# Performance work log

Hardware: AMD Instinct MI355X
Metric: run time of the kernel (lower is better)

## Reference

```python
import jax, jax.numpy as jnp
import numpy as np

H, W = 8, 8
N = 1 + H * W          # 65 tokens (cls + patches)
DIM = 128
HEADS = 8
DH = 32
INNER = HEADS * DH     # 256
B = 64
EPS = 1e-5


def setup_inputs() -> dict:
    key = jax.random.key(0)
    ks = jax.random.split(key, 7)
    x = jax.random.normal(ks[0], (B, N, DIM), dtype=jnp.float32)
    gamma = jnp.ones((DIM,), jnp.float32)
    beta = jnp.zeros((DIM,), jnp.float32)
    # kaiming_uniform-ish init scale for linear weights
    s_qk = float(np.sqrt(1.0 / DIM))
    Wqk = jax.random.uniform(ks[1], (DIM, 2 * INNER), jnp.float32, -s_qk, s_qk)
    # per-(query, key)-position value weights: [n, n, dim, inner]
    Wv = jax.random.uniform(ks[2], (N, N, DIM, INNER), jnp.float32, -s_qk, s_qk)
    s_o = float(np.sqrt(1.0 / INNER))
    Wout = jax.random.uniform(ks[3], (INNER, DIM), jnp.float32, -s_o, s_o)
    bout = jax.random.uniform(ks[4], (DIM,), jnp.float32, -s_o, s_o)
    return {"x": x, "gamma": gamma, "beta": beta, "Wqk": Wqk, "Wv": Wv,
            "Wout": Wout, "bout": bout}


def reference(x, gamma, beta, Wqk, Wv, Wout, bout):
    b, n, d = x.shape
    # LayerNorm
    mu = jnp.mean(x, axis=-1, keepdims=True)
    var = jnp.mean(jnp.square(x - mu), axis=-1, keepdims=True)
    xn = (x - mu) / jnp.sqrt(var + EPS) * gamma + beta
    # q, k projections
    qk = xn @ Wqk                               # [b, n, 2*inner]
    q, k = jnp.split(qk, 2, axis=-1)
    q = q.reshape(b, n, HEADS, DH).transpose(0, 2, 1, 3)  # [b, h, n, dh]
    k = k.reshape(b, n, HEADS, DH).transpose(0, 2, 1, 3)
    scale = DH ** -0.5
    dots = jnp.einsum('bhnd,bhmd->bhnm', q, k) * scale
    attn = jax.nn.softmax(dots, axis=-1)        # [b, h, n, m]
    # per-(n,m) value: v[b,n,m] = xn[b,n] @ Wv[n,m]  -> [b, n, m, inner]
    v = jnp.einsum('bnd,nmde->bnme', xn, Wv)
    v = v.reshape(b, n, n, HEADS, DH)           # [b, n, m, h, dh]
    # weighted sum over keys m
    out = jnp.einsum('bhnm,bnmhd->bnhd', attn, v).reshape(b, n, INNER)
    return out @ Wout + bout
```

## Files before the change

### kernel.cpp

```cpp
#include <hip/hip_runtime.h>

#define EPS 1e-5f

typedef __attribute__((ext_vector_type(8))) short short8;
typedef __attribute__((ext_vector_type(4))) float float4v;

__device__ __forceinline__ unsigned short f2bf(float x) {
  unsigned int u = __builtin_bit_cast(unsigned int, x);
  u += 0x7fffu + ((u >> 16) & 1u);
  return (unsigned short)(u >> 16);
}
__device__ __forceinline__ float bf2f(unsigned short h) {
  unsigned int u = ((unsigned int)h) << 16;
  return __builtin_bit_cast(float, u);
}

__global__ __launch_bounds__(256) void ln_kernel(
    const float* __restrict__ x, const float* __restrict__ gamma,
    const float* __restrict__ beta, float* __restrict__ xn,
    float* __restrict__ inner) {
  {
    const int zi = blockIdx.x * 1024 + threadIdx.x * 4;
    float4 z; z.x = 0.f; z.y = 0.f; z.z = 0.f; z.w = 0.f;
    *(float4*)(inner + zi) = z;
  }
  const int row = blockIdx.x * 4 + (threadIdx.x >> 6);
  const int lane = threadIdx.x & 63;
  const float2 v = ((const float2*)(x + (size_t)row * 128))[lane];
  float s = v.x + v.y;
#pragma unroll
  for (int off = 1; off < 64; off <<= 1) s += __shfl_xor(s, off);
  const float mu = s * (1.f / 128.f);
  const float dx = v.x - mu, dy = v.y - mu;
  float qv = dx * dx + dy * dy;
#pragma unroll
  for (int off = 1; off < 64; off <<= 1) qv += __shfl_xor(qv, off);
  const float rstd = 1.f / sqrtf(qv * (1.f / 128.f) + EPS);
  const float2 g = ((const float2*)gamma)[lane];
  const float2 be = ((const float2*)beta)[lane];
  float2 o;
  o.x = dx * rstd * g.x + be.x;
  o.y = dy * rstd * g.y + be.y;
  ((float2*)(xn + (size_t)row * 128))[lane] = o;
}

__global__ __launch_bounds__(256) void qk_kernel(
    const float* __restrict__ xn, const float* __restrict__ Wqk,
    float* __restrict__ qk) {
  __shared__ float xsx[32][130];
  __shared__ float wsx[128][68];
  const int t = threadIdx.x;
  const int r0 = blockIdx.x * 32, c0 = blockIdx.y * 64;
  for (int i = t; i < 32 * 32; i += 256) {
    int r = i >> 5, c = (i & 31) << 2;
    float4 v = *(const float4*)(xn + (size_t)(r0 + r) * 128 + c);
    float* dst = &xsx[r][c];
    dst[0] = v.x; dst[1] = v.y; dst[2] = v.z; dst[3] = v.w;
  }
  for (int i = t; i < 128 * 16; i += 256) {
    int k = i >> 4, c = (i & 15) << 2;
    *(float4*)&wsx[k][c] = *(const float4*)(Wqk + (size_t)k * 512 + c0 + c);
  }
  __syncthreads();
  const int rr = (t >> 4) * 2, cc = (t & 15) * 4;
  float acc[2][4] = {{0.f, 0.f, 0.f, 0.f}, {0.f, 0.f, 0.f, 0.f}};
  for (int k = 0; k < 128; k++) {
    float4 wv4 = *(const float4*)&wsx[k][cc];
    float x0 = xsx[rr][k], x1 = xsx[rr + 1][k];
    acc[0][0] += x0 * wv4.x; acc[0][1] += x0 * wv4.y;
    acc[0][2] += x0 * wv4.z; acc[0][3] += x0 * wv4.w;
    acc[1][0] += x1 * wv4.x; acc[1][1] += x1 * wv4.y;
    acc[1][2] += x1 * wv4.z; acc[1][3] += x1 * wv4.w;
  }
#pragma unroll
  for (int r = 0; r < 2; r++) {
    float4 o;
    o.x = acc[r][0]; o.y = acc[r][1]; o.z = acc[r][2]; o.w = acc[r][3];
    *(float4*)(qk + (size_t)(r0 + rr + r) * 512 + c0 + cc) = o;
  }
}

__global__ __launch_bounds__(256) void softmax_kernel(
    const float* __restrict__ qk, float* __restrict__ attn) {
  const int b = blockIdx.x >> 3, h = blockIdx.x & 7;
  __shared__ float qs[65][33];
  __shared__ float ks[65][33];
  __shared__ float dotsS[65][66];
  __shared__ float rsum[65];
  const int t = threadIdx.x;
  for (int i = t; i < 65 * 32; i += 256) {
    int n = i >> 5, d = i & 31;
    size_t base = ((size_t)b * 65 + n) * 512 + h * 32 + d;
    qs[n][d] = qk[base];
    ks[n][d] = qk[base + 256];
  }
  __syncthreads();
  const float scale = 0.17677669529663687f;
  for (int i = t; i < 65 * 65; i += 256) {
    int n = i / 65, mm = i - n * 65;
    float s = 0.f;
#pragma unroll
    for (int d = 0; d < 32; d++) s += qs[n][d] * ks[mm][d];
    dotsS[n][mm] = s * scale;
  }
  __syncthreads();
  if (t < 65) {
    float mx = -1e30f;
    for (int mm = 0; mm < 65; mm++) mx = fmaxf(mx, dotsS[t][mm]);
    float sum = 0.f;
    for (int mm = 0; mm < 65; mm++) {
      float e = __expf(dotsS[t][mm] - mx);
      dotsS[t][mm] = e;
      sum += e;
    }
    rsum[t] = 1.f / sum;
  }
  __syncthreads();
  const size_t obase = ((size_t)b * 8 + h) * 65 * 65;
  for (int i = t; i < 65 * 65; i += 256) {
    int n = i / 65;
    attn[obase + i] = dotsS[n][i - n * 65] * rsum[n];
  }
}

__global__ __launch_bounds__(256, 4) void attnv_kernel(
    const float* __restrict__ xn, const float* __restrict__ attn,
    const float* __restrict__ Wv, float* __restrict__ inner) {
  __shared__ __align__(16) char sbuf[33280];
  __shared__ float attnL[17 * 65];
  float* xs = (float*)sbuf;
  unsigned short* wvb = (unsigned short*)sbuf;

  const int nq = blockIdx.x >> 3, h = blockIdx.x & 7;
  const int mc = blockIdx.y;
  const int ms = (mc == 0) ? 0 : (17 + (mc - 1) * 16);
  const int cnt = (mc == 0) ? 17 : 16;

  const int t = threadIdx.x, lane = t & 63, w = t >> 6;
  const int boff = w * 16;
  const int er = lane & 15, q = lane >> 4;

  const int e = t & 31;
  const int d0 = (t >> 5) * 16;
  const int kc0 = d0 >> 3;
  const float* wbase = Wv + (size_t)nq * 65 * 32768 + (size_t)ms * 32768
                          + (size_t)h * 32 + e;

  float stg[16];
  {
    const float* p = wbase + (size_t)d0 * 256;
#pragma unroll
    for (int i = 0; i < 16; i++) stg[i] = __builtin_nontemporal_load(p + (size_t)i * 256);
  }

  for (int i = t; i < cnt * 64; i += 256) {
    int mloc = i >> 6, b = i & 63;
    attnL[mloc * 65 + b] =
        attn[(((size_t)b * 8 + h) * 65 + nq) * 65 + ms + mloc];
  }
  for (int i = t; i < 64 * 32; i += 256) {
    int b = i >> 5, c = (i & 31) << 2;
    float4 v = *(const float4*)(xn + ((size_t)b * 65 + nq) * 128 + c);
    float* dst = xs + b * 130 + c;
    dst[0] = v.x; dst[1] = v.y; dst[2] = v.z; dst[3] = v.w;
  }
  __syncthreads();

  short8 ah[4], al[4];
  {
    const int arow = boff + er;
#pragma unroll
    for (int s = 0; s < 4; s++) {
#pragma unroll
      for (int j = 0; j < 8; j++) {
        float xv = xs[arow * 130 + s * 32 + q * 8 + j];
        unsigned short hi = f2bf(xv);
        ah[s][j] = (short)hi;
        al[s][j] = (short)f2bf(xv - bf2f(hi));
      }
    }
  }
  __syncthreads();

  {
    short8 w0, w1;
#pragma unroll
    for (int j = 0; j < 8; j++) {
      w0[j] = (short)f2bf(stg[j]);
      w1[j] = (short)f2bf(stg[8 + j]);
    }
    *(short8*)&wvb[e * 128 + ((kc0 ^ (e & 15)) << 3)] = w0;
    *(short8*)&wvb[e * 128 + (((kc0 + 1) ^ (e & 15)) << 3)] = w1;
  }
  __syncthreads();

  float4v acc0 = {0.f, 0.f, 0.f, 0.f}, acc1 = {0.f, 0.f, 0.f, 0.f};

  for (int i = 0; i < cnt; i++) {
    const int cur = i & 1;
    if (i + 1 < cnt) {
      const float* p = wbase + (size_t)(i + 1) * 32768 + (size_t)d0 * 256;
#pragma unroll
      for (int j = 0; j < 16; j++) stg[j] = __builtin_nontemporal_load(p + (size_t)j * 256);
    }
    const unsigned short* wb = wvb + cur * 4096;
    float4v P0 = {0.f, 0.f, 0.f, 0.f}, P1 = {0.f, 0.f, 0.f, 0.f};
    __builtin_amdgcn_s_setprio(1);
#pragma unroll
    for (int s = 0; s < 4; s++) {
      const int kc = 4 * s + q;
      short8 b0 = *(const short8*)&wb[er * 128 + ((kc ^ er) << 3)];
      short8 b1 = *(const short8*)&wb[(er + 16) * 128 + ((kc ^ er) << 3)];
      P0 = __builtin_amdgcn_mfma_f32_16x16x32_bf16(ah[s], b0, P0, 0, 0, 0);
      P1 = __builtin_amdgcn_mfma_f32_16x16x32_bf16(ah[s], b1, P1, 0, 0, 0);
      P0 = __builtin_amdgcn_mfma_f32_16x16x32_bf16(al[s], b0, P0, 0, 0, 0);
      P1 = __builtin_amdgcn_mfma_f32_16x16x32_bf16(al[s], b1, P1, 0, 0, 0);
    }
    __builtin_amdgcn_s_setprio(0);
    {
      const float* ap = attnL + i * 65 + boff + q * 4;
#pragma unroll
      for (int r = 0; r < 4; r++) {
        float av = ap[r];
        acc0[r] += av * P0[r];
        acc1[r] += av * P1[r];
      }
    }
    if (i + 1 < cnt) {
      short8 w0, w1;
#pragma unroll
      for (int j = 0; j < 8; j++) {
        w0[j] = (short)f2bf(stg[j]);
        w1[j] = (short)f2bf(stg[8 + j]);
      }
      unsigned short* wbw = wvb + (1 - cur) * 4096;
      *(short8*)&wbw[e * 128 + ((kc0 ^ (e & 15)) << 3)] = w0;
      *(short8*)&wbw[e * 128 + (((kc0 + 1) ^ (e & 15)) << 3)] = w1;
    }
    __syncthreads();
  }

#pragma unroll
  for (int r = 0; r < 4; r++) {
    int b = boff + q * 4 + r;
    size_t o = ((size_t)b * 65 + nq) * 256 + h * 32;
    atomicAdd(inner + o + er, acc0[r]);
    atomicAdd(inner + o + 16 + er, acc1[r]);
  }
}

__global__ __launch_bounds__(256) void outproj_kernel(
    const float* __restrict__ inner, const float* __restrict__ Wout,
    const float* __restrict__ bout, float* __restrict__ out) {
  __shared__ float isx[16][258];
  __shared__ float wsx[64][132];
  const int t = threadIdx.x;
  const int r0 = blockIdx.x * 16;
  for (int i = t; i < 16 * 64; i += 256) {
    int r = i >> 6, c = (i & 63) << 2;
    float4 v = *(const float4*)(inner + (size_t)(r0 + r) * 256 + c);
    float* dst = &isx[r][c];
    dst[0] = v.x; dst[1] = v.y; dst[2] = v.z; dst[3] = v.w;
  }
  const int rr = (t >> 5) * 2, cc = (t & 31) * 4;
  float acc[2][4] = {{0.f, 0.f, 0.f, 0.f}, {0.f, 0.f, 0.f, 0.f}};
  for (int kc = 0; kc < 4; kc++) {
    __syncthreads();
    for (int i = t; i < 64 * 32; i += 256) {
      int k = i >> 5, c = (i & 31) << 2;
      *(float4*)&wsx[k][c] = *(const float4*)(Wout + (size_t)(kc * 64 + k) * 128 + c);
    }
    __syncthreads();
#pragma unroll 8
    for (int k = 0; k < 64; k++) {
      float4 wv4 = *(const float4*)&wsx[k][cc];
      float x0 = isx[rr][kc * 64 + k];
      float x1 = isx[rr + 1][kc * 64 + k];
      acc[0][0] += x0 * wv4.x; acc[0][1] += x0 * wv4.y;
      acc[0][2] += x0 * wv4.z; acc[0][3] += x0 * wv4.w;
      acc[1][0] += x1 * wv4.x; acc[1][1] += x1 * wv4.y;
      acc[1][2] += x1 * wv4.z; acc[1][3] += x1 * wv4.w;
    }
  }
  float4 bb = *(const float4*)(bout + cc);
#pragma unroll
  for (int r = 0; r < 2; r++) {
    float4 o;
    o.x = acc[r][0] + bb.x; o.y = acc[r][1] + bb.y;
    o.z = acc[r][2] + bb.z; o.w = acc[r][3] + bb.w;
    *(float4*)(out + (size_t)(r0 + rr + r) * 128 + cc) = o;
  }
}

extern "C" void kernel_launch(void* const* d_in, const int* in_sizes, int n_in,
                              void* d_out, int out_size, void* d_ws, size_t ws_size,
                              hipStream_t stream) {
  const float* x     = (const float*)d_in[0];
  const float* gamma = (const float*)d_in[1];
  const float* beta  = (const float*)d_in[2];
  const float* Wqk   = (const float*)d_in[3];
  const float* Wv    = (const float*)d_in[4];
  const float* Wout  = (const float*)d_in[5];
  const float* bout  = (const float*)d_in[6];
  float* out = (float*)d_out;
  float* ws  = (float*)d_ws;

  float* xn    = ws;
  float* qk    = ws + 532480;
  float* attn  = ws + 2662400;
  float* inner = ws + 4825600;

  ln_kernel<<<1040, 256, 0, stream>>>(x, gamma, beta, xn, inner);
  qk_kernel<<<dim3(130, 8), 256, 0, stream>>>(xn, Wqk, qk);
  softmax_kernel<<<512, 256, 0, stream>>>(qk, attn);
  attnv_kernel<<<dim3(520, 4), 256, 0, stream>>>(xn, attn, Wv, inner);
  outproj_kernel<<<260, 256, 0, stream>>>(inner, Wout, bout, out);
}
```

Before: 774.1 us.

## Restructure attn-v kernel so each block covers all heads for one query

Each attn-v block now handles one query position across all 8 heads, instead of one (query, head) pair, using 512 threads and a 16-way split over keys. Each Wv slice is fetched as contiguous 1KB rows of 256 floats rather than 128-byte pieces, and the converted xn fragments are reused across all heads. Every thread keeps 64 loads in flight to deepen the prefetch of the bandwidth-bound Wv stream. In exchange it uses 128KB of LDS per block and many more registers per thread, which limits occupancy to about one block per CU and risks register spilling.

```diff
diff --git a/kernel.cpp b/kernel.cpp
--- a/kernel.cpp
+++ b/kernel.cpp
@@ -123,42 +123,62 @@
   }
 }
 
-__global__ __launch_bounds__(256, 4) void attnv_kernel(
+__global__ __launch_bounds__(512, 2) void attnv_kernel(
     const float* __restrict__ xn, const float* __restrict__ attn,
     const float* __restrict__ Wv, float* __restrict__ inner) {
-  __shared__ __align__(16) char sbuf[33280];
-  __shared__ float attnL[17 * 65];
+  __shared__ __align__(16) char sbuf[131072];
+  __shared__ float attnL[5 * 8 * 64];
   float* xs = (float*)sbuf;
   unsigned short* wvb = (unsigned short*)sbuf;
 
-  const int nq = blockIdx.x >> 3, h = blockIdx.x & 7;
+  const int nq = blockIdx.x;
   const int mc = blockIdx.y;
-  const int ms = (mc == 0) ? 0 : (17 + (mc - 1) * 16);
-  const int cnt = (mc == 0) ? 17 : 16;
-
-  const int t = threadIdx.x, lane = t & 63, w = t >> 6;
-  const int boff = w * 16;
+  const int ms = (mc * 65) >> 4;
+  const int cnt = (((mc + 1) * 65) >> 4) - ms;
+
+  const int t = threadIdx.x;
+  const int lane = t & 63;
+  const int w = t >> 6;
   const int er = lane & 15, q = lane >> 4;
-
-  const int e = t & 31;
-  const int d0 = (t >> 5) * 16;
-  const int kc0 = d0 >> 3;
-  const float* wbase = Wv + (size_t)nq * 65 * 32768 + (size_t)ms * 32768
-                          + (size_t)h * 32 + e;
-
-  float stg[16];
-  {
-    const float* p = wbase + (size_t)d0 * 256;
-#pragma unroll
-    for (int i = 0; i < 16; i++) stg[i] = __builtin_nontemporal_load(p + (size_t)i * 256);
-  }
-
-  for (int i = t; i < cnt * 64; i += 256) {
-    int mloc = i >> 6, b = i & 63;
-    attnL[mloc * 65 + b] =
-        attn[(((size_t)b * 8 + h) * 65 + nq) * 65 + ms + mloc];
-  }
-  for (int i = t; i < 64 * 32; i += 256) {
+  const int rg = w & 1, cg = w >> 1;
+
+  const int eS = t & 255;
+  const int dS0 = (t >> 8) << 6;
+  const float* wq = Wv + ((size_t)nq * 65 + ms) * 32768 + (size_t)dS0 * 256 + eS;
+
+  float stg[64];
+
+#define ISSUE(mm) do {                                                        \
+    const float* p_ = wq + (size_t)(mm) * 32768;                              \
+    _Pragma("unroll")                                                         \
+    for (int i_ = 0; i_ < 64; i_++)                                           \
+      stg[i_] = __builtin_nontemporal_load(p_ + (size_t)i_ * 256);            \
+  } while (0)
+
+#define CONVWRITE(buf) do {                                                   \
+    unsigned short* wb_ = wvb + (size_t)(buf) * 32768 + eS * 128;             \
+    const int cb_ = (t >> 8) << 3;                                            \
+    _Pragma("unroll")                                                         \
+    for (int jj_ = 0; jj_ < 8; jj_++) {                                       \
+      short8 pk_;                                                             \
+      _Pragma("unroll")                                                       \
+      for (int j_ = 0; j_ < 8; j_++) pk_[j_] = (short)f2bf(stg[jj_ * 8 + j_]);\
+      *(short8*)&wb_[((cb_ + jj_) ^ (eS & 15)) << 3] = pk_;                   \
+    }                                                                         \
+  } while (0)
+
+  ISSUE(0);
+
+  const int tot = cnt << 9;
+  for (int i = t; i < tot; i += 512) {
+    int mloc = i % cnt;
+    int rest = i / cnt;
+    int h = rest & 7;
+    int b = rest >> 3;
+    attnL[(mloc * 8 + h) * 64 + b] =
+        attn[(((size_t)(b * 8 + h) * 65) + nq) * 65 + ms + mloc];
+  }
+  for (int i = t; i < 64 * 32; i += 512) {
     int b = i >> 5, c = (i & 31) << 2;
     float4 v = *(const float4*)(xn + ((size_t)b * 65 + nq) * 128 + c);
     float* dst = xs + b * 130 + c;
@@ -166,86 +186,84 @@
   }
   __syncthreads();
 
-  short8 ah[4], al[4];
-  {
-    const int arow = boff + er;
+  short8 ah[2][4], al[2][4];
+#pragma unroll
+  for (int rt = 0; rt < 2; rt++) {
+    const int arow = rg * 32 + rt * 16 + er;
 #pragma unroll
     for (int s = 0; s < 4; s++) {
 #pragma unroll
       for (int j = 0; j < 8; j++) {
         float xv = xs[arow * 130 + s * 32 + q * 8 + j];
         unsigned short hi = f2bf(xv);
-        ah[s][j] = (short)hi;
-        al[s][j] = (short)f2bf(xv - bf2f(hi));
+        ah[rt][s][j] = (short)hi;
+        al[rt][s][j] = (short)f2bf(xv - bf2f(hi));
       }
     }
   }
   __syncthreads();
 
-  {
-    short8 w0, w1;
-#pragma unroll
-    for (int j = 0; j < 8; j++) {
-      w0[j] = (short)f2bf(stg[j]);
-      w1[j] = (short)f2bf(stg[8 + j]);
-    }
-    *(short8*)&wvb[e * 128 + ((kc0 ^ (e & 15)) << 3)] = w0;
-    *(short8*)&wvb[e * 128 + (((kc0 + 1) ^ (e & 15)) << 3)] = w1;
-  }
-  __syncthreads();
-
-  float4v acc0 = {0.f, 0.f, 0.f, 0.f}, acc1 = {0.f, 0.f, 0.f, 0.f};
+  CONVWRITE(0);
+  __syncthreads();
+
+  float4v acc[2][4];
+#pragma unroll
+  for (int rt = 0; rt < 2; rt++)
+#pragma unroll
+    for (int ct = 0; ct < 4; ct++)
+      acc[rt][ct] = (float4v){0.f, 0.f, 0.f, 0.f};
 
   for (int i = 0; i < cnt; i++) {
-    const int cur = i & 1;
-    if (i + 1 < cnt) {
-      const float* p = wbase + (size_t)(i + 1) * 32768 + (size_t)d0 * 256;
-#pragma unroll
-      for (int j = 0; j < 16; j++) stg[j] = __builtin_nontemporal_load(p + (size_t)j * 256);
-    }
-    const unsigned short* wb = wvb + cur * 4096;
-    float4v P0 = {0.f, 0.f, 0.f, 0.f}, P1 = {0.f, 0.f, 0.f, 0.f};
+    if (i + 1 < cnt) ISSUE(i + 1);
+    const unsigned short* wb = wvb + (size_t)(i & 1) * 32768;
+    float4v P[2][4];
+#pragma unroll
+    for (int rt = 0; rt < 2; rt++)
+#pragma unroll
+      for (int ct = 0; ct < 4; ct++)
+        P[rt][ct] = (float4v){0.f, 0.f, 0.f, 0.f};
     __builtin_amdgcn_s_setprio(1);
 #pragma unroll
     for (int s = 0; s < 4; s++) {
       const int kc = 4 * s + q;
-      short8 b0 = *(const short8*)&wb[er * 128 + ((kc ^ er) << 3)];
-      short8 b1 = *(const short8*)&wb[(er + 16) * 128 + ((kc ^ er) << 3)];
-      P0 = __builtin_amdgcn_mfma_f32_16x16x32_bf16(ah[s], b0, P0, 0, 0, 0);
-      P1 = __builtin_amdgcn_mfma_f32_16x16x32_bf16(ah[s], b1, P1, 0, 0, 0);
-      P0 = __builtin_amdgcn_mfma_f32_16x16x32_bf16(al[s], b0, P0, 0, 0, 0);
-      P1 = __builtin_amdgcn_mfma_f32_16x16x32_bf16(al[s], b1, P1, 0, 0, 0);
+#pragma unroll
+      for (int ct = 0; ct < 4; ct++) {
+        short8 bf = *(const short8*)&wb[(cg * 64 + ct * 16 + er) * 128 + ((kc ^ er) << 3)];
+        P[0][ct] = __builtin_amdgcn_mfma_f32_16x16x32_bf16(ah[0][s], bf, P[0][ct], 0, 0, 0);
+        P[0][ct] = __builtin_amdgcn_mfma_f32_16x16x32_bf16(al[0][s], bf, P[0][ct], 0, 0, 0);
+        P[1][ct] = __builtin_amdgcn_mfma_f32_16x16x32_bf16(ah[1][s], bf, P[1][ct], 0, 0, 0);
+        P[1][ct] = __builtin_amdgcn_mfma_f32_16x16x32_bf16(al[1][s], bf, P[1][ct], 0, 0, 0);
+      }
     }
     __builtin_amdgcn_s_setprio(0);
-    {
-      const float* ap = attnL + i * 65 + boff + q * 4;
+#pragma unroll
+    for (int rt = 0; rt < 2; rt++) {
+#pragma unroll
+      for (int ct = 0; ct < 4; ct++) {
+        const int h = cg * 2 + (ct >> 1);
+        const float* ap = attnL + (i * 8 + h) * 64 + rg * 32 + rt * 16 + q * 4;
+#pragma unroll
+        for (int r = 0; r < 4; r++) acc[rt][ct][r] += ap[r] * P[rt][ct][r];
+      }
+    }
+    if (i + 1 < cnt) CONVWRITE((i + 1) & 1);
+    __syncthreads();
+  }
+
+#undef ISSUE
+#undef CONVWRITE
+
+#pragma unroll
+  for (int rt = 0; rt < 2; rt++) {
+#pragma unroll
+    for (int ct = 0; ct < 4; ct++) {
+      const int ecol = cg * 64 + ct * 16 + er;
 #pragma unroll
       for (int r = 0; r < 4; r++) {
-        float av = ap[r];
-        acc0[r] += av * P0[r];
-        acc1[r] += av * P1[r];
+        const int b = rg * 32 + rt * 16 + q * 4 + r;
+        atomicAdd(inner + ((size_t)b * 65 + nq) * 256 + ecol, acc[rt][ct][r]);
       }
     }
-    if (i + 1 < cnt) {
-      short8 w0, w1;
-#pragma unroll
-      for (int j = 0; j < 8; j++) {
-        w0[j] = (short)f2bf(stg[j]);
-        w1[j] = (short)f2bf(stg[8 + j]);
-      }
-      unsigned short* wbw = wvb + (1 - cur) * 4096;
-      *(short8*)&wbw[e * 128 + ((kc0 ^ (e & 15)) << 3)] = w0;
-      *(short8*)&wbw[e * 128 + (((kc0 + 1) ^ (e & 15)) << 3)] = w1;
-    }
-    __syncthreads();
-  }
-
-#pragma unroll
-  for (int r = 0; r < 4; r++) {
-    int b = boff + q * 4 + r;
-    size_t o = ((size_t)b * 65 + nq) * 256 + h * 32;
-    atomicAdd(inner + o + er, acc0[r]);
-    atomicAdd(inner + o + 16 + er, acc1[r]);
   }
 }
 
@@ -313,6 +331,6 @@
   ln_kernel<<<1040, 256, 0, stream>>>(x, gamma, beta, xn, inner);
   qk_kernel<<<dim3(130, 8), 256, 0, stream>>>(xn, Wqk, qk);
   softmax_kernel<<<512, 256, 0, stream>>>(qk, attn);
-  attnv_kernel<<<dim3(520, 4), 256, 0, stream>>>(xn, attn, Wv, inner);
+  attnv_kernel<<<dim3(65, 16), 512, 0, stream>>>(xn, attn, Wv, inner);
   outproj_kernel<<<260, 256, 0, stream>>>(inner, Wout, bout, out);
 }
```

Result: slower. 806.0 us (+4.1%).
